# Kernel optimization log

Measured on AMD Instinct MI355X. Metric: run time of the kernel, lower is better.

The kernel has to match this reference:

```python
import jax, jax.numpy as jnp
import numpy as np

EMBED = 768
HEADS = 12


def setup_inputs() -> dict:
    key = jax.random.key(0)
    k1, k2, k3, k4, k5 = jax.random.split(key, 5)
    B, N, E = 8, 1024, EMBED
    x = jax.random.normal(k1, (B, N, E), dtype=jnp.float32)
    # torch Linear stored as [in, out] here (math-equivalent: y = x @ W + b)
    w_qkv = jax.random.normal(k2, (E, 3 * E), dtype=jnp.float32) * (E ** -0.5)
    b_qkv = jax.random.normal(k3, (3 * E,), dtype=jnp.float32) * 0.02
    w_proj = jax.random.normal(k4, (E, E), dtype=jnp.float32) * (E ** -0.5)
    b_proj = jax.random.normal(k5, (E,), dtype=jnp.float32) * 0.02
    return {"x": x, "w_qkv": w_qkv, "b_qkv": b_qkv, "w_proj": w_proj, "b_proj": b_proj}


def reference(x, w_qkv, b_qkv, w_proj, b_proj):
    B, N, E = x.shape
    H = HEADS
    D = E // H
    qkv = x @ w_qkv + b_qkv                       # [B, N, 3E]
    # rearrange 'b n (h d qkv) -> qkv b h n d': qkv index is innermost in last dim
    qkv = qkv.reshape(B, N, H, D, 3)
    qkv = jnp.transpose(qkv, (4, 0, 2, 1, 3))      # [3, B, H, N, D]
    q, k, v = qkv[0], qkv[1], qkv[2]
    energy = jnp.einsum('bhqd,bhkd->bhqk', q, k)   # [B, H, N, N]
    scaling = float(E) ** 0.5
    # NOTE: original scales AFTER softmax (unusual but faithful)
    att = jax.nn.softmax(energy, axis=-1) / scaling
    # dropout_prob = 0.0 -> identity
    out = jnp.einsum('bhqk,bhkd->bhqd', att, v)    # [B, H, N, D]
    out = jnp.transpose(out, (0, 2, 1, 3)).reshape(B, N, E)
    return out @ w_proj + b_proj
```

## Files before the change

### kernel.cpp

```cpp
#include <hip/hip_runtime.h>
#include <hip/hip_bf16.h>
#include <stdint.h>

#define NSEQ 1024
#define EMB 768
#define HEADS 12
#define HD 64
#define BATCH 8
#define BHN (BATCH*HEADS)

typedef __attribute__((ext_vector_type(8))) short bf16x8;
typedef __attribute__((ext_vector_type(4))) short bf16x4;
typedef __attribute__((ext_vector_type(4))) float f32x4;

typedef const void __attribute__((address_space(1))) cglobal_void;
typedef void __attribute__((address_space(3))) lds_void_t;

#define LOG2E 1.4426950408889634f

__device__ __forceinline__ void load_lds16(const void* g, void* l) {
    __builtin_amdgcn_global_load_lds((cglobal_void*)g, (lds_void_t*)l, 16, 0, 0);
}

__device__ __forceinline__ unsigned short f2bf(float f) {
    __hip_bfloat16 h = __float2bfloat16(f);
    return *reinterpret_cast<unsigned short*>(&h);
}

__device__ __forceinline__ unsigned int cvt_pk_bf16(float lo, float hi) {
    unsigned int r;
    asm("v_cvt_pk_bf16_f32 %0, %1, %2" : "=v"(r) : "v"(lo), "v"(hi));
    return r;
}

__device__ __forceinline__ float exp2_hw(float x) {
#if __has_builtin(__builtin_amdgcn_exp2f)
    return __builtin_amdgcn_exp2f(x);
#else
    return exp2f(x);
#endif
}

__global__ void conv_x_kernel(const float* __restrict__ x, unsigned short* __restrict__ xb) {
    int i = (blockIdx.x * 256 + threadIdx.x) * 4;
    float4 v = *reinterpret_cast<const float4*>(x + i);
    ushort4 o;
    o.x = f2bf(v.x); o.y = f2bf(v.y); o.z = f2bf(v.z); o.w = f2bf(v.w);
    *reinterpret_cast<ushort4*>(xb + i) = o;
}

template <int PERM>
__global__ void transpose_w_kernel(const float* __restrict__ w, unsigned short* __restrict__ wt,
                                   int K, int C) {
    __shared__ unsigned short tile[64][65];
    int c0 = blockIdx.x * 64;
    int k0 = blockIdx.y * 64;
    int t = threadIdx.x;
    int r = t >> 2, cc = (t & 3) * 16;
#pragma unroll
    for (int e = 0; e < 16; e += 4) {
        float4 v = *reinterpret_cast<const float4*>(w + (size_t)(k0 + r) * C + c0 + cc + e);
        float s0 = (PERM && ((c0 + cc + e + 0) % 3 == 0)) ? LOG2E : 1.0f;
        float s1 = (PERM && ((c0 + cc + e + 1) % 3 == 0)) ? LOG2E : 1.0f;
        float s2 = (PERM && ((c0 + cc + e + 2) % 3 == 0)) ? LOG2E : 1.0f;
        float s3 = (PERM && ((c0 + cc + e + 3) % 3 == 0)) ? LOG2E : 1.0f;
        tile[r][cc + e + 0] = f2bf(v.x * s0);
        tile[r][cc + e + 1] = f2bf(v.y * s1);
        tile[r][cc + e + 2] = f2bf(v.z * s2);
        tile[r][cc + e + 3] = f2bf(v.w * s3);
    }
    __syncthreads();
    int c = t >> 2, kk0 = (t & 3) * 16;
    int cg = c0 + c;
    int n;
    if (PERM) {
        int qkv = cg % 3, h = cg / 192, d = (cg % 192) / 3;
        n = qkv * EMB + h * HD + d;
    } else {
        n = cg;
    }
    uint4 lo, hi;
    lo.x = (unsigned)tile[kk0 + 0][c] | ((unsigned)tile[kk0 + 1][c] << 16);
    lo.y = (unsigned)tile[kk0 + 2][c] | ((unsigned)tile[kk0 + 3][c] << 16);
    lo.z = (unsigned)tile[kk0 + 4][c] | ((unsigned)tile[kk0 + 5][c] << 16);
    lo.w = (unsigned)tile[kk0 + 6][c] | ((unsigned)tile[kk0 + 7][c] << 16);
    hi.x = (unsigned)tile[kk0 + 8][c] | ((unsigned)tile[kk0 + 9][c] << 16);
    hi.y = (unsigned)tile[kk0 + 10][c] | ((unsigned)tile[kk0 + 11][c] << 16);
    hi.z = (unsigned)tile[kk0 + 12][c] | ((unsigned)tile[kk0 + 13][c] << 16);
    hi.w = (unsigned)tile[kk0 + 14][c] | ((unsigned)tile[kk0 + 15][c] << 16);
    *reinterpret_cast<uint4*>(wt + (size_t)n * K + k0 + kk0) = lo;
    *reinterpret_cast<uint4*>(wt + (size_t)n * K + k0 + kk0 + 8) = hi;
}

__global__ void perm_bias_kernel(const float* __restrict__ b, float* __restrict__ bp) {
    int c = blockIdx.x * 256 + threadIdx.x;
    int qkv = c % 3, h = c / 192, d = (c % 192) / 3;
    bp[qkv * EMB + h * HD + d] = (qkv == 0) ? b[c] * LOG2E : b[c];
}

__launch_bounds__(256, 4)
__global__ void gemm_qkv_kernel(const unsigned short* __restrict__ A,
                                const unsigned short* __restrict__ Bt,
                                const float* __restrict__ bias,
                                unsigned short* __restrict__ qout,
                                unsigned short* __restrict__ kout,
                                unsigned short* __restrict__ vout) {
    constexpr int TN = 18;
    constexpr int NWG = 64 * TN;
    constexpr int CHUNK = NWG / 8;
    constexpr int K = EMB;
    __shared__ unsigned short lds_a[128 * 64];
    __shared__ unsigned short lds_b[128 * 64];
    int bx0 = blockIdx.x;
    int bx = (bx0 % 8) * CHUNK + bx0 / 8;
    int tm = bx / TN, tn = bx % TN;
    bool vpath = (tn >= 12);
    const unsigned short* Bt_eff = Bt + (vpath ? (size_t)1536 * K : (size_t)0);
    const float* bias_eff = bias + (vpath ? 1536 : 0);
    int n0 = (vpath ? tn - 12 : tn) * 128;
    int m0 = tm * 128;
    int t = threadIdx.x;
    int l = t & 63;
    int g = l >> 4, c16 = l & 15;
    int wr = (t >> 7) & 1, wc = (t >> 6) & 1;
    int wbase = (t & 192);

    const char* baseA_f = vpath ? (const char*)lds_b : (const char*)lds_a;
    const char* baseB_f = vpath ? (const char*)lds_a : (const char*)lds_b;
    int roA = (vpath ? wc : wr) * 64;
    int roB = (vpath ? wr : wc) * 64;

    f32x4 acc[4][4];
#pragma unroll
    for (int i = 0; i < 4; i++)
#pragma unroll
        for (int j = 0; j < 4; j++)
#pragma unroll
            for (int r = 0; r < 4; r++) acc[i][j][r] = 0.f;

    for (int kt = 0; kt < K; kt += 64) {
        __syncthreads();
#pragma unroll
        for (int i = 0; i < 4; i++) {
            int c = i * 256 + t;
            int row = c >> 3;
            int sc = ((c & 7) ^ (row & 7)) * 8;
            load_lds16(A + (size_t)(m0 + row) * K + kt + sc, lds_a + (size_t)(i * 256 + wbase) * 8);
            load_lds16(Bt_eff + (size_t)(n0 + row) * K + kt + sc, lds_b + (size_t)(i * 256 + wbase) * 8);
        }
        __syncthreads();
#pragma unroll
        for (int kk = 0; kk < 2; kk++) {
            int cb = kk * 64 + g * 16;
            bf16x8 fa[4], fb[4];
#pragma unroll
            for (int i = 0; i < 4; i++) {
                int row = roA + i * 16 + c16;
                fa[i] = *reinterpret_cast<const bf16x8*>(
                    baseA_f + row * 128 + (cb ^ ((row & 7) << 4)));
            }
#pragma unroll
            for (int j = 0; j < 4; j++) {
                int row = roB + j * 16 + c16;
                fb[j] = *reinterpret_cast<const bf16x8*>(
                    baseB_f + row * 128 + (cb ^ ((row & 7) << 4)));
            }
#pragma unroll
            for (int i = 0; i < 4; i++)
#pragma unroll
                for (int j = 0; j < 4; j++)
                    acc[i][j] = __builtin_amdgcn_mfma_f32_16x16x32_bf16(fa[i], fb[j], acc[i][j], 0, 0, 0);
        }
    }

    if (vpath) {
#pragma unroll
        for (int i = 0; i < 4; i++) {
#pragma unroll
            for (int r = 0; r < 4; r++) {
                int nv = wc * 64 + i * 16 + (g * 4) + r + n0;
                float bv = bias_eff[nv];
                int hh = nv >> 6, dd = nv & 63;
#pragma unroll
                for (int j = 0; j < 4; j++) {
                    int m_g = m0 + wr * 64 + j * 16 + c16;
                    int bb = m_g >> 10, nn = m_g & 1023;
                    int nnp = (nn & ~31) | ((nn & 12) << 1) | ((nn >> 2) & 4) | (nn & 3);
                    vout[((size_t)(bb * HEADS + hh) * HD + dd) * NSEQ + nnp] =
                        f2bf(acc[i][j][r] + bv);
                }
            }
        }
    } else {
#pragma unroll
        for (int i = 0; i < 4; i++) {
            int mbase = m0 + wr * 64 + i * 16 + (g * 4);
#pragma unroll
            for (int j = 0; j < 4; j++) {
                int n_g = n0 + wc * 64 + j * 16 + c16;
                float bv = bias_eff[n_g];
#pragma unroll
                for (int r = 0; r < 4; r++) {
                    int m_g = mbase + r;
                    float v = acc[i][j][r] + bv;
                    int rem = n_g - ((n_g >= 768) ? 768 : 0);
                    int hh = rem >> 6, dd = rem & 63;
                    int bb = m_g >> 10, nn = m_g & 1023;
                    if (n_g < 768)
                        qout[(size_t)((bb * HEADS + hh) * NSEQ + nn) * HD + dd] = f2bf(v);
                    else
                        kout[(size_t)((bb * HEADS + hh) * NSEQ + nn) * HD + dd] = f2bf(v);
                }
            }
        }
    }
}

__launch_bounds__(256, 4)
__global__ void proj_kernel(const unsigned short* __restrict__ A,
                            const unsigned short* __restrict__ Bt,
                            const float* __restrict__ bias,
                            float* __restrict__ out) {
    constexpr int TN = 6;
    constexpr int NWG = 128 * TN;
    constexpr int CHUNK = NWG / 8;
    constexpr int K = EMB;
    __shared__ unsigned short lds_a[64 * 64];
    __shared__ unsigned short lds_b[128 * 64];
    int bx0 = blockIdx.x;
    int bx = (bx0 % 8) * CHUNK + bx0 / 8;
    int tm = bx / TN, tn = bx % TN;
    int m0 = tm * 64, n0 = tn * 128;
    int t = threadIdx.x;
    int l = t & 63;
    int g = l >> 4, c16 = l & 15;
    int w = t >> 6;
    int wbase = (t & 192);

    f32x4 acc[4][2];
#pragma unroll
    for (int i = 0; i < 4; i++)
#pragma unroll
        for (int j = 0; j < 2; j++)
#pragma unroll
            for (int r = 0; r < 4; r++) acc[i][j][r] = 0.f;

    for (int kt = 0; kt < K; kt += 64) {
        __syncthreads();
#pragma unroll
        for (int i = 0; i < 2; i++) {
            int c = i * 256 + t;
            int row = c >> 3;
            int sc = ((c & 7) ^ (row & 7)) * 8;
            load_lds16(A + (size_t)(m0 + row) * K + kt + sc, lds_a + (size_t)(i * 256 + wbase) * 8);
        }
#pragma unroll
        for (int i = 0; i < 4; i++) {
            int c = i * 256 + t;
            int row = c >> 3;
            int sc = ((c & 7) ^ (row & 7)) * 8;
            load_lds16(Bt + (size_t)(n0 + row) * K + kt + sc, lds_b + (size_t)(i * 256 + wbase) * 8);
        }
        __syncthreads();
#pragma unroll
        for (int kk = 0; kk < 2; kk++) {
            int cb = kk * 64 + g * 16;
            bf16x8 fa[4], fb[2];
#pragma unroll
            for (int i = 0; i < 4; i++) {
                int row = i * 16 + c16;
                fa[i] = *reinterpret_cast<const bf16x8*>(
                    (const char*)lds_a + row * 128 + (cb ^ ((row & 7) << 4)));
            }
#pragma unroll
            for (int j = 0; j < 2; j++) {
                int row = w * 32 + j * 16 + c16;
                fb[j] = *reinterpret_cast<const bf16x8*>(
                    (const char*)lds_b + row * 128 + (cb ^ ((row & 7) << 4)));
            }
#pragma unroll
            for (int i = 0; i < 4; i++)
#pragma unroll
                for (int j = 0; j < 2; j++)
                    acc[i][j] = __builtin_amdgcn_mfma_f32_16x16x32_bf16(fa[i], fb[j], acc[i][j], 0, 0, 0);
        }
    }

#pragma unroll
    for (int i = 0; i < 4; i++) {
        int mbase = m0 + i * 16 + g * 4;
#pragma unroll
        for (int j = 0; j < 2; j++) {
            int n_g = n0 + w * 32 + j * 16 + c16;
            float bv = bias[n_g];
#pragma unroll
            for (int r = 0; r < 4; r++)
                out[(size_t)(mbase + r) * EMB + n_g] = acc[i][j][r] + bv;
        }
    }
}

__launch_bounds__(256, 3)
__global__ void attn_kernel(const unsigned short* __restrict__ Q,
                            const unsigned short* __restrict__ K,
                            const unsigned short* __restrict__ Vt,
                            unsigned short* __restrict__ Oout) {
    __shared__ unsigned short k_lds[2][64 * 64];
    __shared__ unsigned short vt_lds[2][64 * 64];
    int bx = blockIdx.x;
    int bh = bx % BHN;
    int q0 = (bx / BHN) << 7;
    int b = bh / HEADS, h = bh % HEADS;
    int t = threadIdx.x, w = t >> 6, l = t & 63;
    int g = l >> 4, c16 = l & 15;
    const unsigned short* Qh = Q + (size_t)bh * NSEQ * HD;
    const unsigned short* Kh = K + (size_t)bh * NSEQ * HD;
    const unsigned short* Vth = Vt + (size_t)bh * NSEQ * HD;

    int qrA = q0 + w * 32 + c16;
    int qrB = qrA + 16;
    bf16x8 qfA[2], qfB[2];
    qfA[0] = *reinterpret_cast<const bf16x8*>(Qh + (size_t)qrA * HD + g * 8);
    qfA[1] = *reinterpret_cast<const bf16x8*>(Qh + (size_t)qrA * HD + 32 + g * 8);
    qfB[0] = *reinterpret_cast<const bf16x8*>(Qh + (size_t)qrB * HD + g * 8);
    qfB[1] = *reinterpret_cast<const bf16x8*>(Qh + (size_t)qrB * HD + 32 + g * 8);

    float lA = 0.f, lB = 0.f;
    f32x4 accA[4], accB[4];
#pragma unroll
    for (int jd = 0; jd < 4; jd++)
#pragma unroll
        for (int r = 0; r < 4; r++) { accA[jd][r] = 0.f; accB[jd][r] = 0.f; }

    auto stage = [&](int buf, int kv) {
#pragma unroll
        for (int i = 0; i < 2; i++) {
            int tt = i * 256 + t;
            int row = tt >> 3;
            int sc = ((tt & 7) ^ (row & 7)) * 8;
            load_lds16(Kh + (size_t)(kv + row) * HD + sc, k_lds[buf] + (size_t)(tt & ~63) * 8);
            load_lds16(Vth + (size_t)row * NSEQ + kv + sc, vt_lds[buf] + (size_t)(tt & ~63) * 8);
        }
    };

    stage(0, 0);
    __syncthreads();
    int cur = 0;
    for (int it = 0; it < 16; ++it) {
        if (it < 15) stage(cur ^ 1, (it + 1) << 6);

        const char* kbase = (const char*)k_lds[cur];
        const char* vbase = (const char*)vt_lds[cur];

        f32x4 stA[4], stB[4];
#pragma unroll
        for (int jk = 0; jk < 4; jk++)
#pragma unroll
            for (int r = 0; r < 4; r++) { stA[jk][r] = 0.f; stB[jk][r] = 0.f; }
        __builtin_amdgcn_s_setprio(1);
#pragma unroll
        for (int kk = 0; kk < 2; kk++) {
            int cb = kk * 64 + g * 16;
#pragma unroll
            for (int jk = 0; jk < 4; jk++) {
                int row = jk * 16 + c16;
                bf16x8 kf = *reinterpret_cast<const bf16x8*>(
                    kbase + row * 128 + (cb ^ ((row & 7) << 4)));
                stA[jk] = __builtin_amdgcn_mfma_f32_16x16x32_bf16(kf, qfA[kk], stA[jk], 0, 0, 0);
                stB[jk] = __builtin_amdgcn_mfma_f32_16x16x32_bf16(kf, qfB[kk], stB[jk], 0, 0, 0);
            }
        }
        __builtin_amdgcn_s_setprio(0);

#pragma unroll
        for (int jk = 0; jk < 4; jk++)
#pragma unroll
            for (int r = 0; r < 4; r++) {
                stA[jk][r] = exp2_hw(stA[jk][r]);
                stB[jk][r] = exp2_hw(stB[jk][r]);
            }

        union PU { unsigned int u[4]; bf16x8 v; };
        PU puA0, puA1, puB0, puB1;
#pragma unroll
        for (int p = 0; p < 2; p++) {
            puA0.u[p]     = cvt_pk_bf16(stA[0][2 * p], stA[0][2 * p + 1]);
            puA0.u[2 + p] = cvt_pk_bf16(stA[1][2 * p], stA[1][2 * p + 1]);
            puA1.u[p]     = cvt_pk_bf16(stA[2][2 * p], stA[2][2 * p + 1]);
            puA1.u[2 + p] = cvt_pk_bf16(stA[3][2 * p], stA[3][2 * p + 1]);
            puB0.u[p]     = cvt_pk_bf16(stB[0][2 * p], stB[0][2 * p + 1]);
            puB0.u[2 + p] = cvt_pk_bf16(stB[1][2 * p], stB[1][2 * p + 1]);
            puB1.u[p]     = cvt_pk_bf16(stB[2][2 * p], stB[2][2 * p + 1]);
            puB1.u[2 + p] = cvt_pk_bf16(stB[3][2 * p], stB[3][2 * p + 1]);
        }
        bf16x8 pfA[2] = {puA0.v, puA1.v};
        bf16x8 pfB[2] = {puB0.v, puB1.v};

        __builtin_amdgcn_s_setprio(1);
#pragma unroll
        for (int ks = 0; ks < 2; ks++) {
            int cb = ks * 64 + g * 16;
#pragma unroll
            for (int jd = 0; jd < 4; jd++) {
                int row = jd * 16 + c16;
                bf16x8 vf = *reinterpret_cast<const bf16x8*>(
                    vbase + row * 128 + (cb ^ ((row & 7) << 4)));
                accA[jd] = __builtin_amdgcn_mfma_f32_16x16x32_bf16(vf, pfA[ks], accA[jd], 0, 0, 0);
                accB[jd] = __builtin_amdgcn_mfma_f32_16x16x32_bf16(vf, pfB[ks], accB[jd], 0, 0, 0);
            }
        }
        __builtin_amdgcn_s_setprio(0);

        lA += (((stA[0][0] + stA[0][1]) + (stA[0][2] + stA[0][3])) +
               ((stA[1][0] + stA[1][1]) + (stA[1][2] + stA[1][3]))) +
              (((stA[2][0] + stA[2][1]) + (stA[2][2] + stA[2][3])) +
               ((stA[3][0] + stA[3][1]) + (stA[3][2] + stA[3][3])));
        lB += (((stB[0][0] + stB[0][1]) + (stB[0][2] + stB[0][3])) +
               ((stB[1][0] + stB[1][1]) + (stB[1][2] + stB[1][3]))) +
              (((stB[2][0] + stB[2][1]) + (stB[2][2] + stB[2][3])) +
               ((stB[3][0] + stB[3][1]) + (stB[3][2] + stB[3][3])));

        __syncthreads();
        cur ^= 1;
    }

    lA += __shfl_xor(lA, 16);
    lA += __shfl_xor(lA, 32);
    lB += __shfl_xor(lB, 16);
    lB += __shfl_xor(lB, 32);
    const float scale = 27.712812921102035f;
    float invA = 1.0f / (lA * scale);
    float invB = 1.0f / (lB * scale);
    size_t qbaseA = ((size_t)(b * NSEQ + qrA) * HEADS + h) * HD;
    size_t qbaseB = ((size_t)(b * NSEQ + qrB) * HEADS + h) * HD;
#pragma unroll
    for (int jd = 0; jd < 4; jd++)
#pragma unroll
        for (int r = 0; r < 4; r++) {
            int d = jd * 16 + g * 4 + r;
            Oout[qbaseA + d] = f2bf(accA[jd][r] * invA);
            Oout[qbaseB + d] = f2bf(accB[jd][r] * invB);
        }
}

extern "C" void kernel_launch(void* const* d_in, const int* in_sizes, int n_in,
                              void* d_out, int out_size, void* d_ws, size_t ws_size,
                              hipStream_t stream) {
    const float* x = (const float*)d_in[0];
    const float* w_qkv = (const float*)d_in[1];
    const float* b_qkv = (const float*)d_in[2];
    const float* w_proj = (const float*)d_in[3];
    const float* b_proj = (const float*)d_in[4];

    char* ws = (char*)d_ws;
    unsigned short* xb      = (unsigned short*)(ws + 0);
    unsigned short* wt_qkv  = (unsigned short*)(ws + 12582912);
    unsigned short* wt_proj = (unsigned short*)(ws + 16121856);
    float*          biasp   = (float*)(ws + 17301504);
    unsigned short* qb      = (unsigned short*)(ws + 17310720);
    unsigned short* kb      = (unsigned short*)(ws + 29893632);
    unsigned short* vtb     = (unsigned short*)(ws + 42476544);
    unsigned short* ao      = (unsigned short*)(ws + 55059456);

    conv_x_kernel<<<6144, 256, 0, stream>>>(x, xb);
    transpose_w_kernel<1><<<dim3(36, 12), 256, 0, stream>>>(w_qkv, wt_qkv, EMB, 3 * EMB);
    transpose_w_kernel<0><<<dim3(12, 12), 256, 0, stream>>>(w_proj, wt_proj, EMB, EMB);
    perm_bias_kernel<<<9, 256, 0, stream>>>(b_qkv, biasp);

    gemm_qkv_kernel<<<64 * 18, 256, 0, stream>>>(xb, wt_qkv, biasp, qb, kb, vtb);
    attn_kernel<<<BHN * 8, 256, 0, stream>>>(qb, kb, vtb, ao);
    proj_kernel<<<128 * 6, 256, 0, stream>>>(ao, wt_proj, b_proj, (float*)d_out);
}
```

Before: 103.7 us.

## Merge prep kernels into one launch and load attention K/V directly from global

The four preprocessing launches (x conversion, two weight transposes, bias permutation) become a single prep kernel that branches on block index, removing launch gaps. The attention kernel drops its double-buffered LDS staging of K and V^T and the per-iteration barrier. Each lane now reads its MFMA fragments straight from global memory (through cache), and the row sum is accumulated as a vector. This removes LDS traffic and synchronisation, but exposes global-load latency with no explicit prefetch. Each K/V tile is also re-read by all four waves from cache.

```diff
diff --git a/kernel.cpp b/kernel.cpp
--- a/kernel.cpp
+++ b/kernel.cpp
@@ -10,7 +10,6 @@
 #define BHN (BATCH*HEADS)
 
 typedef __attribute__((ext_vector_type(8))) short bf16x8;
-typedef __attribute__((ext_vector_type(4))) short bf16x4;
 typedef __attribute__((ext_vector_type(4))) float f32x4;
 
 typedef const void __attribute__((address_space(1))) cglobal_void;
@@ -41,61 +40,72 @@
 #endif
 }
 
-__global__ void conv_x_kernel(const float* __restrict__ x, unsigned short* __restrict__ xb) {
-    int i = (blockIdx.x * 256 + threadIdx.x) * 4;
-    float4 v = *reinterpret_cast<const float4*>(x + i);
-    ushort4 o;
-    o.x = f2bf(v.x); o.y = f2bf(v.y); o.z = f2bf(v.z); o.w = f2bf(v.w);
-    *reinterpret_cast<ushort4*>(xb + i) = o;
-}
-
-template <int PERM>
-__global__ void transpose_w_kernel(const float* __restrict__ w, unsigned short* __restrict__ wt,
-                                   int K, int C) {
+__global__ void prep_kernel(const float* __restrict__ x, unsigned short* __restrict__ xb,
+                            const float* __restrict__ w_qkv, unsigned short* __restrict__ wt_qkv,
+                            const float* __restrict__ w_proj, unsigned short* __restrict__ wt_proj,
+                            const float* __restrict__ b_qkv, float* __restrict__ biasp) {
     __shared__ unsigned short tile[64][65];
-    int c0 = blockIdx.x * 64;
-    int k0 = blockIdx.y * 64;
-    int t = threadIdx.x;
-    int r = t >> 2, cc = (t & 3) * 16;
-#pragma unroll
-    for (int e = 0; e < 16; e += 4) {
-        float4 v = *reinterpret_cast<const float4*>(w + (size_t)(k0 + r) * C + c0 + cc + e);
-        float s0 = (PERM && ((c0 + cc + e + 0) % 3 == 0)) ? LOG2E : 1.0f;
-        float s1 = (PERM && ((c0 + cc + e + 1) % 3 == 0)) ? LOG2E : 1.0f;
-        float s2 = (PERM && ((c0 + cc + e + 2) % 3 == 0)) ? LOG2E : 1.0f;
-        float s3 = (PERM && ((c0 + cc + e + 3) % 3 == 0)) ? LOG2E : 1.0f;
-        tile[r][cc + e + 0] = f2bf(v.x * s0);
-        tile[r][cc + e + 1] = f2bf(v.y * s1);
-        tile[r][cc + e + 2] = f2bf(v.z * s2);
-        tile[r][cc + e + 3] = f2bf(v.w * s3);
-    }
-    __syncthreads();
-    int c = t >> 2, kk0 = (t & 3) * 16;
-    int cg = c0 + c;
-    int n;
-    if (PERM) {
-        int qkv = cg % 3, h = cg / 192, d = (cg % 192) / 3;
-        n = qkv * EMB + h * HD + d;
-    } else {
-        n = cg;
-    }
-    uint4 lo, hi;
-    lo.x = (unsigned)tile[kk0 + 0][c] | ((unsigned)tile[kk0 + 1][c] << 16);
-    lo.y = (unsigned)tile[kk0 + 2][c] | ((unsigned)tile[kk0 + 3][c] << 16);
-    lo.z = (unsigned)tile[kk0 + 4][c] | ((unsigned)tile[kk0 + 5][c] << 16);
-    lo.w = (unsigned)tile[kk0 + 6][c] | ((unsigned)tile[kk0 + 7][c] << 16);
-    hi.x = (unsigned)tile[kk0 + 8][c] | ((unsigned)tile[kk0 + 9][c] << 16);
-    hi.y = (unsigned)tile[kk0 + 10][c] | ((unsigned)tile[kk0 + 11][c] << 16);
-    hi.z = (unsigned)tile[kk0 + 12][c] | ((unsigned)tile[kk0 + 13][c] << 16);
-    hi.w = (unsigned)tile[kk0 + 14][c] | ((unsigned)tile[kk0 + 15][c] << 16);
-    *reinterpret_cast<uint4*>(wt + (size_t)n * K + k0 + kk0) = lo;
-    *reinterpret_cast<uint4*>(wt + (size_t)n * K + k0 + kk0 + 8) = hi;
-}
-
-__global__ void perm_bias_kernel(const float* __restrict__ b, float* __restrict__ bp) {
-    int c = blockIdx.x * 256 + threadIdx.x;
-    int qkv = c % 3, h = c / 192, d = (c % 192) / 3;
-    bp[qkv * EMB + h * HD + d] = (qkv == 0) ? b[c] * LOG2E : b[c];
+    int bx = blockIdx.x, t = threadIdx.x;
+    if (bx < 6144) {
+        int i = (bx * 256 + t) * 4;
+        float4 v = *reinterpret_cast<const float4*>(x + i);
+        ushort4 o;
+        o.x = f2bf(v.x); o.y = f2bf(v.y); o.z = f2bf(v.z); o.w = f2bf(v.w);
+        *reinterpret_cast<ushort4*>(xb + i) = o;
+        return;
+    }
+    if (bx < 6720) {
+        bool perm = (bx < 6576);
+        int bb = perm ? bx - 6144 : bx - 6576;
+        int tilesC = perm ? 36 : 12;
+        int C = perm ? 3 * EMB : EMB;
+        const float* w = perm ? w_qkv : w_proj;
+        unsigned short* wt = perm ? wt_qkv : wt_proj;
+        int c0 = (bb % tilesC) * 64, k0 = (bb / tilesC) * 64;
+        int r = t >> 2, cc = (t & 3) * 16;
+#pragma unroll
+        for (int e = 0; e < 16; e += 4) {
+            float4 v = *reinterpret_cast<const float4*>(w + (size_t)(k0 + r) * C + c0 + cc + e);
+            float s0 = (perm && ((c0 + cc + e + 0) % 3 == 0)) ? LOG2E : 1.0f;
+            float s1 = (perm && ((c0 + cc + e + 1) % 3 == 0)) ? LOG2E : 1.0f;
+            float s2 = (perm && ((c0 + cc + e + 2) % 3 == 0)) ? LOG2E : 1.0f;
+            float s3 = (perm && ((c0 + cc + e + 3) % 3 == 0)) ? LOG2E : 1.0f;
+            tile[r][cc + e + 0] = f2bf(v.x * s0);
+            tile[r][cc + e + 1] = f2bf(v.y * s1);
+            tile[r][cc + e + 2] = f2bf(v.z * s2);
+            tile[r][cc + e + 3] = f2bf(v.w * s3);
+        }
+        __syncthreads();
+        int c = t >> 2, kk0 = (t & 3) * 16;
+        int cg = c0 + c;
+        int n;
+        if (perm) {
+            int qkv = cg % 3, h = cg / 192, d = (cg % 192) / 3;
+            n = qkv * EMB + h * HD + d;
+        } else {
+            n = cg;
+        }
+        uint4 lo, hi;
+        lo.x = (unsigned)tile[kk0 + 0][c] | ((unsigned)tile[kk0 + 1][c] << 16);
+        lo.y = (unsigned)tile[kk0 + 2][c] | ((unsigned)tile[kk0 + 3][c] << 16);
+        lo.z = (unsigned)tile[kk0 + 4][c] | ((unsigned)tile[kk0 + 5][c] << 16);
+        lo.w = (unsigned)tile[kk0 + 6][c] | ((unsigned)tile[kk0 + 7][c] << 16);
+        hi.x = (unsigned)tile[kk0 + 8][c] | ((unsigned)tile[kk0 + 9][c] << 16);
+        hi.y = (unsigned)tile[kk0 + 10][c] | ((unsigned)tile[kk0 + 11][c] << 16);
+        hi.z = (unsigned)tile[kk0 + 12][c] | ((unsigned)tile[kk0 + 13][c] << 16);
+        hi.w = (unsigned)tile[kk0 + 14][c] | ((unsigned)tile[kk0 + 15][c] << 16);
+        *reinterpret_cast<uint4*>(wt + (size_t)n * EMB + k0 + kk0) = lo;
+        *reinterpret_cast<uint4*>(wt + (size_t)n * EMB + k0 + kk0 + 8) = hi;
+        return;
+    }
+    {
+        int c = (bx - 6720) * 256 + t;
+        if (c < 3 * EMB) {
+            int qkv = c % 3, h = c / 192, d = (c % 192) / 3;
+            biasp[qkv * EMB + h * HD + d] = (qkv == 0) ? b_qkv[c] * LOG2E : b_qkv[c];
+        }
+        return;
+    }
 }
 
 __launch_bounds__(256, 4)
@@ -305,8 +315,6 @@
                             const unsigned short* __restrict__ K,
                             const unsigned short* __restrict__ Vt,
                             unsigned short* __restrict__ Oout) {
-    __shared__ unsigned short k_lds[2][64 * 64];
-    __shared__ unsigned short vt_lds[2][64 * 64];
     int bx = blockIdx.x;
     int bh = bx % BHN;
     int q0 = (bx / BHN) << 7;
@@ -325,32 +333,31 @@
     qfB[0] = *reinterpret_cast<const bf16x8*>(Qh + (size_t)qrB * HD + g * 8);
     qfB[1] = *reinterpret_cast<const bf16x8*>(Qh + (size_t)qrB * HD + 32 + g * 8);
 
-    float lA = 0.f, lB = 0.f;
+    const unsigned short* Kf = Kh + (size_t)c16 * HD + g * 8;
+    const unsigned short* Vf = Vth + (size_t)c16 * NSEQ + g * 8;
+
+    f32x4 lAv, lBv;
+#pragma unroll
+    for (int r = 0; r < 4; r++) { lAv[r] = 0.f; lBv[r] = 0.f; }
     f32x4 accA[4], accB[4];
 #pragma unroll
     for (int jd = 0; jd < 4; jd++)
 #pragma unroll
         for (int r = 0; r < 4; r++) { accA[jd][r] = 0.f; accB[jd][r] = 0.f; }
 
-    auto stage = [&](int buf, int kv) {
-#pragma unroll
-        for (int i = 0; i < 2; i++) {
-            int tt = i * 256 + t;
-            int row = tt >> 3;
-            int sc = ((tt & 7) ^ (row & 7)) * 8;
-            load_lds16(Kh + (size_t)(kv + row) * HD + sc, k_lds[buf] + (size_t)(tt & ~63) * 8);
-            load_lds16(Vth + (size_t)row * NSEQ + kv + sc, vt_lds[buf] + (size_t)(tt & ~63) * 8);
-        }
-    };
-
-    stage(0, 0);
-    __syncthreads();
-    int cur = 0;
+    union PU { unsigned int u[4]; bf16x8 v; };
+
+#pragma unroll 1
     for (int it = 0; it < 16; ++it) {
-        if (it < 15) stage(cur ^ 1, (it + 1) << 6);
-
-        const char* kbase = (const char*)k_lds[cur];
-        const char* vbase = (const char*)vt_lds[cur];
+        int kv = it << 6;
+
+        bf16x8 kf[2][4];
+#pragma unroll
+        for (int kk = 0; kk < 2; kk++)
+#pragma unroll
+            for (int jk = 0; jk < 4; jk++)
+                kf[kk][jk] = *reinterpret_cast<const bf16x8*>(
+                    Kf + (size_t)(kv + jk * 16) * HD + kk * 32);
 
         f32x4 stA[4], stB[4];
 #pragma unroll
@@ -359,17 +366,12 @@
             for (int r = 0; r < 4; r++) { stA[jk][r] = 0.f; stB[jk][r] = 0.f; }
         __builtin_amdgcn_s_setprio(1);
 #pragma unroll
-        for (int kk = 0; kk < 2; kk++) {
-            int cb = kk * 64 + g * 16;
+        for (int kk = 0; kk < 2; kk++)
 #pragma unroll
             for (int jk = 0; jk < 4; jk++) {
-                int row = jk * 16 + c16;
-                bf16x8 kf = *reinterpret_cast<const bf16x8*>(
-                    kbase + row * 128 + (cb ^ ((row & 7) << 4)));
-                stA[jk] = __builtin_amdgcn_mfma_f32_16x16x32_bf16(kf, qfA[kk], stA[jk], 0, 0, 0);
-                stB[jk] = __builtin_amdgcn_mfma_f32_16x16x32_bf16(kf, qfB[kk], stB[jk], 0, 0, 0);
-            }
-        }
+                stA[jk] = __builtin_amdgcn_mfma_f32_16x16x32_bf16(kf[kk][jk], qfA[kk], stA[jk], 0, 0, 0);
+                stB[jk] = __builtin_amdgcn_mfma_f32_16x16x32_bf16(kf[kk][jk], qfB[kk], stB[jk], 0, 0, 0);
+            }
         __builtin_amdgcn_s_setprio(0);
 
 #pragma unroll
@@ -379,8 +381,6 @@
                 stA[jk][r] = exp2_hw(stA[jk][r]);
                 stB[jk][r] = exp2_hw(stB[jk][r]);
             }
-
-        union PU { unsigned int u[4]; bf16x8 v; };
         PU puA0, puA1, puB0, puB1;
 #pragma unroll
         for (int p = 0; p < 2; p++) {
@@ -395,35 +395,28 @@
         }
         bf16x8 pfA[2] = {puA0.v, puA1.v};
         bf16x8 pfB[2] = {puB0.v, puB1.v};
-
-        __builtin_amdgcn_s_setprio(1);
+        lAv += (stA[0] + stA[1]) + (stA[2] + stA[3]);
+        lBv += (stB[0] + stB[1]) + (stB[2] + stB[3]);
+
 #pragma unroll
         for (int ks = 0; ks < 2; ks++) {
-            int cb = ks * 64 + g * 16;
+            bf16x8 vf[4];
+#pragma unroll
+            for (int jd = 0; jd < 4; jd++)
+                vf[jd] = *reinterpret_cast<const bf16x8*>(
+                    Vf + (size_t)(jd * 16) * NSEQ + kv + ks * 32);
+            __builtin_amdgcn_s_setprio(1);
 #pragma unroll
             for (int jd = 0; jd < 4; jd++) {
-                int row = jd * 16 + c16;
-                bf16x8 vf = *reinterpret_cast<const bf16x8*>(
-                    vbase + row * 128 + (cb ^ ((row & 7) << 4)));
-                accA[jd] = __builtin_amdgcn_mfma_f32_16x16x32_bf16(vf, pfA[ks], accA[jd], 0, 0, 0);
-                accB[jd] = __builtin_amdgcn_mfma_f32_16x16x32_bf16(vf, pfB[ks], accB[jd], 0, 0, 0);
-            }
-        }
-        __builtin_amdgcn_s_setprio(0);
-
-        lA += (((stA[0][0] + stA[0][1]) + (stA[0][2] + stA[0][3])) +
-               ((stA[1][0] + stA[1][1]) + (stA[1][2] + stA[1][3]))) +
-              (((stA[2][0] + stA[2][1]) + (stA[2][2] + stA[2][3])) +
-               ((stA[3][0] + stA[3][1]) + (stA[3][2] + stA[3][3])));
-        lB += (((stB[0][0] + stB[0][1]) + (stB[0][2] + stB[0][3])) +
-               ((stB[1][0] + stB[1][1]) + (stB[1][2] + stB[1][3]))) +
-              (((stB[2][0] + stB[2][1]) + (stB[2][2] + stB[2][3])) +
-               ((stB[3][0] + stB[3][1]) + (stB[3][2] + stB[3][3])));
-
-        __syncthreads();
-        cur ^= 1;
-    }
-
+                accA[jd] = __builtin_amdgcn_mfma_f32_16x16x32_bf16(vf[jd], pfA[ks], accA[jd], 0, 0, 0);
+                accB[jd] = __builtin_amdgcn_mfma_f32_16x16x32_bf16(vf[jd], pfB[ks], accB[jd], 0, 0, 0);
+            }
+            __builtin_amdgcn_s_setprio(0);
+        }
+    }
+
+    float lA = (lAv[0] + lAv[1]) + (lAv[2] + lAv[3]);
+    float lB = (lBv[0] + lBv[1]) + (lBv[2] + lBv[3]);
     lA += __shfl_xor(lA, 16);
     lA += __shfl_xor(lA, 32);
     lB += __shfl_xor(lB, 16);
@@ -462,11 +455,7 @@
     unsigned short* vtb     = (unsigned short*)(ws + 42476544);
     unsigned short* ao      = (unsigned short*)(ws + 55059456);
 
-    conv_x_kernel<<<6144, 256, 0, stream>>>(x, xb);
-    transpose_w_kernel<1><<<dim3(36, 12), 256, 0, stream>>>(w_qkv, wt_qkv, EMB, 3 * EMB);
-    transpose_w_kernel<0><<<dim3(12, 12), 256, 0, stream>>>(w_proj, wt_proj, EMB, EMB);
-    perm_bias_kernel<<<9, 256, 0, stream>>>(b_qkv, biasp);
-
+    prep_kernel<<<6729, 256, 0, stream>>>(x, xb, w_qkv, wt_qkv, w_proj, wt_proj, b_qkv, biasp);
     gemm_qkv_kernel<<<64 * 18, 256, 0, stream>>>(xb, wt_qkv, biasp, qb, kb, vtb);
     attn_kernel<<<BHN * 8, 256, 0, stream>>>(qb, kb, vtb, ao);
     proj_kernel<<<128 * 6, 256, 0, stream>>>(ao, wt_proj, b_proj, (float*)d_out);
```

New measurement: 156.4 us. 1.51x slower.
